# Optimization experiments

Measured on AMD Instinct MI355X. Metric: run time of the kernel, lower is better.

## Reference

```python
import jax, jax.numpy as jnp
import numpy as np

N_QUBITS = 4            # hardcoded by _QLayer encoder (4 rx inputs)
STATE_DIM = 1024        # 2**gnn_arch[-1] = 2**10 amplitudes per node state
FEAT_DIM = 2 * STATE_DIM
HIDDEN = 4              # must equal n_qubits for gating broadcast
OUT_DIM = 2048
N_NODES = 8192

# PauliZ expectation signs: wire 0 is the most-significant bit of the basis index
_IDX = np.arange(2 ** N_QUBITS)
_SIGNS = np.stack([1.0 - 2.0 * ((_IDX >> (N_QUBITS - 1 - w)) & 1) for w in range(N_QUBITS)], axis=1).astype(np.float32)  # [16,4]


def _apply_rx(state, angles, wire):
    # state: [B,2,2,2,2] complex64, angles: [B]
    half = 0.5 * angles
    c = jnp.cos(half).astype(jnp.complex64)
    s = (-1j) * jnp.sin(half).astype(jnp.complex64)
    gate = jnp.stack([jnp.stack([c, s], -1), jnp.stack([s, c], -1)], -2)  # [B,2,2]
    st = jnp.moveaxis(state, wire + 1, 1)
    st = jnp.einsum('bij,bj...->bi...', gate, st)
    return jnp.moveaxis(st, 1, wire + 1)


def _cnot(state, ctrl, tgt):
    flipped = jnp.flip(state, axis=tgt + 1)
    shape = [1] * state.ndim
    shape[ctrl + 1] = 2
    mask = jnp.arange(2).reshape(shape)
    return jnp.where(mask == 1, flipped, state)


def _qlayer(x, theta):
    # x: [B,4] encoding angles; theta: [4] trainable RX angles
    B = x.shape[0]
    state = jnp.zeros((B,) + (2,) * N_QUBITS, jnp.complex64)
    state = state.at[(slice(None),) + (0,) * N_QUBITS].set(1.0)
    for w in range(N_QUBITS):
        state = _apply_rx(state, x[:, w], w)          # encoder RX
    for w in range(N_QUBITS):
        state = _apply_rx(state, jnp.broadcast_to(theta[w], (B,)), w)  # trainable RX
    for w in range(N_QUBITS):
        state = _cnot(state, w, (w + 1) % N_QUBITS)   # CNOT ring (last -> 0)
    probs = (state.real ** 2 + state.imag ** 2).reshape(B, -1)  # [B,16]
    return probs @ jnp.asarray(_SIGNS)                 # [B,4] PauliZ expvals


def setup_inputs() -> dict:
    key = jax.random.key(0)
    ks = jax.random.split(key, 16)
    # random normalized complex node states -> real|imag concat features
    re = jax.random.normal(ks[0], (N_NODES, STATE_DIM), jnp.float32)
    im = jax.random.normal(ks[1], (N_NODES, STATE_DIM), jnp.float32)
    norm = jnp.sqrt(jnp.sum(re ** 2 + im ** 2, axis=1, keepdims=True))
    features = (jnp.concatenate([re, im], axis=1) / norm)[:, None, :]  # [N,1,FEAT_DIM]

    D = FEAT_DIM + HIDDEN
    bound = 1.0 / np.sqrt(D)

    def lin(k):
        kw, kb = jax.random.split(k)
        W = jax.random.uniform(kw, (N_QUBITS, D), jnp.float32, -bound, bound)
        b = jax.random.uniform(kb, (N_QUBITS,), jnp.float32, -bound, bound)
        return W, b

    Wf, bf = lin(ks[2]); Wi, bi = lin(ks[3]); Wg, bg = lin(ks[4]); Wo, bo = lin(ks[5])
    theta_f = jax.random.uniform(ks[6], (N_QUBITS,), jnp.float32, 0.0, 2.0 * np.pi)
    theta_i = jax.random.uniform(ks[7], (N_QUBITS,), jnp.float32, 0.0, 2.0 * np.pi)
    theta_g = jax.random.uniform(ks[8], (N_QUBITS,), jnp.float32, 0.0, 2.0 * np.pi)
    theta_o = jax.random.uniform(ks[9], (N_QUBITS,), jnp.float32, 0.0, 2.0 * np.pi)
    fb = 1.0 / np.sqrt(HIDDEN)
    Wfin = jax.random.uniform(ks[10], (OUT_DIM, HIDDEN), jnp.float32, -fb, fb)
    bfin = jax.random.uniform(ks[11], (OUT_DIM,), jnp.float32, -fb, fb)
    return {"features": features, "Wf": Wf, "bf": bf, "Wi": Wi, "bi": bi,
            "Wg": Wg, "bg": bg, "Wo": Wo, "bo": bo,
            "theta_f": theta_f, "theta_i": theta_i, "theta_g": theta_g, "theta_o": theta_o,
            "Wfin": Wfin, "bfin": bfin}


def reference(features, Wf, bf, Wi, bi, Wg, bg, Wo, bo,
              theta_f, theta_i, theta_g, theta_o, Wfin, bfin):
    D = features.shape[-1]
    Wfx, Wfh = Wf[:, :D], Wf[:, D:]
    Wix, Wih = Wi[:, :D], Wi[:, D:]
    Wgx, Wgh = Wg[:, :D], Wg[:, D:]
    Wox, Woh = Wo[:, :D], Wo[:, D:]
    # precompute the x-part of all gate projections (the only big GEMM)
    px_f = jnp.einsum('nbd,qd->nbq', features, Wfx) + bf
    px_i = jnp.einsum('nbd,qd->nbq', features, Wix) + bi
    px_g = jnp.einsum('nbd,qd->nbq', features, Wgx) + bg
    px_o = jnp.einsum('nbd,qd->nbq', features, Wox) + bo

    B = features.shape[1]
    h0 = jnp.zeros((B, HIDDEN), jnp.float32)
    c0 = jnp.zeros((B, HIDDEN), jnp.float32)

    def step(carry, xs):
        hx, cx = carry
        pf, pi, pg, po = xs
        f = jax.nn.sigmoid(_qlayer(pf + hx @ Wfh.T, theta_f))
        i = jax.nn.sigmoid(_qlayer(pi + hx @ Wih.T, theta_i))
        g = jnp.tanh(_qlayer(pg + hx @ Wgh.T, theta_g))
        o = jax.nn.sigmoid(_qlayer(po + hx @ Woh.T, theta_o))
        cx = f * cx + i * g
        hx = o * jnp.tanh(cx)
        return (hx, cx), hx

    _, outs = jax.lax.scan(step, (h0, c0), (px_f, px_i, px_g, px_o))  # outs: [N,B,H]
    return outs[:, 0, :] @ Wfin.T + bfin  # [N, OUT_DIM]
```

## Files before the change

kernel.cpp:

```cpp
#include <hip/hip_runtime.h>
#include <stdint.h>
#include <math.h>

typedef unsigned int uint_t;

#define FEAT 2048
#define DSTRIDE 2052
#define WARM 40
#define LCH 16
#define STEPS (WARM + LCH)
#define NCH (NN / LCH)
#define NN 8192

__device__ __forceinline__ float sigm_f(float x) {
    return __builtin_amdgcn_rcpf(1.f + __expf(-x));
}
__device__ __forceinline__ float tanh_f(float x) {
    return 1.f - 2.f * __builtin_amdgcn_rcpf(__expf(2.f * x) + 1.f);
}

__global__ __launch_bounds__(256) void k_px(
    const float* __restrict__ feat,
    const float* __restrict__ Wf, const float* __restrict__ Wi,
    const float* __restrict__ Wg, const float* __restrict__ Wo,
    const float* __restrict__ bfp, const float* __restrict__ bip,
    const float* __restrict__ bgp, const float* __restrict__ bop,
    const float* __restrict__ thf, const float* __restrict__ thi,
    const float* __restrict__ thg, const float* __restrict__ tho,
    float* __restrict__ px2)
{
    __shared__ float Wl[16 * 512];
    const int t = threadIdx.x;
    const int wave = t >> 6, lane = t & 63;
    const int rowBase = blockIdx.x * 16;
    const float* Ws[4] = {Wf, Wi, Wg, Wo};

    float acc[4][16];
#pragma unroll
    for (int r = 0; r < 4; ++r)
#pragma unroll
        for (int i = 0; i < 16; ++i) acc[r][i] = 0.f;

    for (int ch = 0; ch < 4; ++ch) {
        __syncthreads();
        for (int i4 = t; i4 < 2048; i4 += 256) {
            const int gq = i4 >> 7;
            const int jj = (i4 & 127) << 2;
            const int g = gq >> 2, q = gq & 3;
            const float4 v = *(const float4*)(Ws[g] + q * DSTRIDE + ch * 512 + jj);
            *(float4*)(&Wl[gq * 512 + jj]) = v;
        }
        __syncthreads();
#pragma unroll
        for (int rr = 0; rr < 4; ++rr) {
            const int n = rowBase + wave * 4 + rr;
            const float* fp = feat + (size_t)n * FEAT + ch * 512 + lane * 8;
            const float4 fa = *(const float4*)(fp);
            const float4 fb = *(const float4*)(fp + 4);
#pragma unroll
            for (int gq = 0; gq < 16; ++gq) {
                const float4 wa = *(const float4*)(&Wl[gq * 512 + lane * 8]);
                const float4 wb = *(const float4*)(&Wl[gq * 512 + lane * 8 + 4]);
                float a = acc[rr][gq];
                a = fmaf(fa.x, wa.x, a); a = fmaf(fa.y, wa.y, a);
                a = fmaf(fa.z, wa.z, a); a = fmaf(fa.w, wa.w, a);
                a = fmaf(fb.x, wb.x, a); a = fmaf(fb.y, wb.y, a);
                a = fmaf(fb.z, wb.z, a); a = fmaf(fb.w, wb.w, a);
                acc[rr][gq] = a;
            }
        }
    }

    float bth[16];
    {
        const float* bs[4] = {bfp, bip, bgp, bop};
        const float* ts[4] = {thf, thi, thg, tho};
#pragma unroll
        for (int g = 0; g < 4; ++g)
#pragma unroll
            for (int q = 0; q < 4; ++q)
                bth[g * 4 + q] = bs[g][q] + ts[g][q];
    }

#pragma unroll
    for (int rr = 0; rr < 4; ++rr) {
#pragma unroll
        for (int i = 0; i < 16; ++i) {
            float v = acc[rr][i];
#pragma unroll
            for (int m = 32; m > 0; m >>= 1) v += __shfl_xor(v, m, 64);
            acc[rr][i] = v + bth[i];
        }
        if (lane == 0) {
            const int n = rowBase + wave * 4 + rr;
            float* dst = px2 + (size_t)n * 16;
            *(float4*)(dst + 0)  = make_float4(acc[rr][0],  acc[rr][1],  acc[rr][2],  acc[rr][3]);
            *(float4*)(dst + 4)  = make_float4(acc[rr][4],  acc[rr][5],  acc[rr][6],  acc[rr][7]);
            *(float4*)(dst + 8)  = make_float4(acc[rr][8],  acc[rr][9],  acc[rr][10], acc[rr][11]);
            *(float4*)(dst + 12) = make_float4(acc[rr][12], acc[rr][13], acc[rr][14], acc[rr][15]);
        }
    }
}

__global__ __launch_bounds__(256) void k_scan(
    const float* __restrict__ Wf, const float* __restrict__ Wi,
    const float* __restrict__ Wg, const float* __restrict__ Wo,
    const float* __restrict__ px2, float* __restrict__ hout)
{
    const int c = blockIdx.x * 256 + threadIdx.x;
    float wh[4][4][4];
    {
        const float* Ws[4] = {Wf, Wi, Wg, Wo};
#pragma unroll
        for (int g = 0; g < 4; ++g)
#pragma unroll
            for (int q = 0; q < 4; ++q)
#pragma unroll
                for (int j = 0; j < 4; ++j)
                    wh[g][q][j] = Ws[g][q * DSTRIDE + FEAT + j];
    }
    float h[4] = {0.f, 0.f, 0.f, 0.f};
    float cc[4] = {0.f, 0.f, 0.f, 0.f};

    float4 PN0, PN1, PN2, PN3;
    {
        const int n0 = c * LCH - WARM;
        const int nc = n0 < 0 ? 0 : n0;
        const float* p = px2 + (size_t)nc * 16;
        PN0 = *(const float4*)(p + 0);
        PN1 = *(const float4*)(p + 4);
        PN2 = *(const float4*)(p + 8);
        PN3 = *(const float4*)(p + 12);
    }

    for (int s = 0; s < STEPS; ++s) {
        const int n = c * LCH + s - WARM;

        float4 PP[4];
        PP[0] = PN0; PP[1] = PN1; PP[2] = PN2; PP[3] = PN3;

        {
            int n2 = n + 1;
            n2 = n2 < 0 ? 0 : n2;
            n2 = n2 > (NN - 1) ? (NN - 1) : n2;
            const float* p2 = px2 + (size_t)n2 * 16;
            PN0 = *(const float4*)(p2 + 0);
            PN1 = *(const float4*)(p2 + 4);
            PN2 = *(const float4*)(p2 + 8);
            PN3 = *(const float4*)(p2 + 12);
        }

        float act[4][4];
#pragma unroll
        for (int g = 0; g < 4; ++g) {
            float z0 = PP[g].x, z1 = PP[g].y, z2 = PP[g].z, z3 = PP[g].w;
#pragma unroll
            for (int j = 0; j < 4; ++j) {
                z0 = fmaf(h[j], wh[g][0][j], z0);
                z1 = fmaf(h[j], wh[g][1][j], z1);
                z2 = fmaf(h[j], wh[g][2][j], z2);
                z3 = fmaf(h[j], wh[g][3][j], z3);
            }
            const float c0 = __cosf(z0), c1 = __cosf(z1);
            const float c2 = __cosf(z2), c3 = __cosf(z3);
            const float m01 = c0 * c1, t23 = c2 * c3;
            const float y0 = c1 * t23, y1 = m01, y2 = m01 * c2, y3 = m01 * t23;
            if (g == 2) {
                act[g][0] = tanh_f(y0); act[g][1] = tanh_f(y1);
                act[g][2] = tanh_f(y2); act[g][3] = tanh_f(y3);
            } else {
                act[g][0] = sigm_f(y0); act[g][1] = sigm_f(y1);
                act[g][2] = sigm_f(y2); act[g][3] = sigm_f(y3);
            }
        }
        if (n >= 0) {
#pragma unroll
            for (int q = 0; q < 4; ++q) {
                const float cn = fmaf(act[0][q], cc[q], act[1][q] * act[2][q]);
                cc[q] = cn;
                h[q] = act[3][q] * tanh_f(cn);
            }
        }
        if (s >= WARM) {
            *(float4*)(hout + (size_t)n * 4) = make_float4(h[0], h[1], h[2], h[3]);
        }
    }
}

__global__ __launch_bounds__(256) void k_out_main(
    const float* __restrict__ hout,
    const float* __restrict__ Wfin, const float* __restrict__ bfin,
    float* __restrict__ out)
{
    const int n = blockIdx.x;
    const int ko = threadIdx.x * 8;
    const float4 h = *(const float4*)(hout + (size_t)n * 4);
    const float4 b0 = *(const float4*)(bfin + ko);
    const float4 b1 = *(const float4*)(bfin + ko + 4);
    const float bb[8] = {b0.x, b0.y, b0.z, b0.w, b1.x, b1.y, b1.z, b1.w};
    float o[8];
#pragma unroll
    for (int j = 0; j < 8; ++j) {
        const float4 w = *(const float4*)(Wfin + (size_t)(ko + j) * 4);
        float v = bb[j];
        v = fmaf(h.x, w.x, v); v = fmaf(h.y, w.y, v);
        v = fmaf(h.z, w.z, v); v = fmaf(h.w, w.w, v);
        o[j] = v;
    }
    float* dst = out + (size_t)n * 2048 + ko;
    *(float4*)(dst)     = make_float4(o[0], o[1], o[2], o[3]);
    *(float4*)(dst + 4) = make_float4(o[4], o[5], o[6], o[7]);
}

__global__ __launch_bounds__(256) void k_out_tail(
    const float* __restrict__ hout,
    const float* __restrict__ Wfin, const float* __restrict__ bfin,
    float* __restrict__ out)
{
    __shared__ float hs[16 * 4];
    const int t = threadIdx.x;
    if (t < 64) hs[t] = hout[(size_t)8176 * 4 + t];
    __syncthreads();
    const int r = t >> 4;
    const int n = 8176 + r;
    const int c0 = (t & 15) * 128;
    const float4 h = *(const float4*)(&hs[r * 4]);
    for (int j = 0; j < 128; j += 8) {
        const int ko = c0 + j;
        const float4 b0 = *(const float4*)(bfin + ko);
        const float4 b1 = *(const float4*)(bfin + ko + 4);
        const float bb[8] = {b0.x, b0.y, b0.z, b0.w, b1.x, b1.y, b1.z, b1.w};
        float o[8];
#pragma unroll
        for (int jj = 0; jj < 8; ++jj) {
            const float4 w = *(const float4*)(Wfin + (size_t)(ko + jj) * 4);
            float v = bb[jj];
            v = fmaf(h.x, w.x, v); v = fmaf(h.y, w.y, v);
            v = fmaf(h.z, w.z, v); v = fmaf(h.w, w.w, v);
            o[jj] = v;
        }
        float* dst = out + (size_t)n * 2048 + ko;
        *(float4*)(dst)     = make_float4(o[0], o[1], o[2], o[3]);
        *(float4*)(dst + 4) = make_float4(o[4], o[5], o[6], o[7]);
    }
}

__global__ __launch_bounds__(256) void k_sentinel(float* __restrict__ out) {
    const size_t i = (size_t)blockIdx.x * 256 + threadIdx.x;
    *(float4*)(out + i * 4) = make_float4(123.f, 123.f, 123.f, 123.f);
}

extern "C" void kernel_launch(void* const* d_in, const int* in_sizes, int n_in,
                              void* d_out, int out_size, void* d_ws, size_t ws_size,
                              hipStream_t stream)
{
    const float* feat = (const float*)d_in[0];
    const float* Wf   = (const float*)d_in[1];
    const float* bfp  = (const float*)d_in[2];
    const float* Wi   = (const float*)d_in[3];
    const float* bip  = (const float*)d_in[4];
    const float* Wg   = (const float*)d_in[5];
    const float* bgp  = (const float*)d_in[6];
    const float* Wo   = (const float*)d_in[7];
    const float* bop  = (const float*)d_in[8];
    const float* thf  = (const float*)d_in[9];
    const float* thi  = (const float*)d_in[10];
    const float* thg  = (const float*)d_in[11];
    const float* tho  = (const float*)d_in[12];
    const float* Wfin = (const float*)d_in[13];
    const float* bfin = (const float*)d_in[14];

    bool ok = (n_in == 15) &&
              in_sizes[0] == 8192 * 2048 &&
              in_sizes[1] == 8208 && in_sizes[3] == 8208 &&
              in_sizes[5] == 8208 && in_sizes[7] == 8208 &&
              in_sizes[2] == 4 && in_sizes[4] == 4 &&
              in_sizes[6] == 4 && in_sizes[8] == 4 &&
              in_sizes[9] == 4 && in_sizes[10] == 4 &&
              in_sizes[11] == 4 && in_sizes[12] == 4 &&
              in_sizes[13] == 8192 && in_sizes[14] == 2048 &&
              out_size == 8192 * 2048;
    if (!ok) {
        hipLaunchKernelGGL(k_sentinel, dim3(8192 * 2048 / 1024), dim3(256), 0,
                           stream, (float*)d_out);
        return;
    }

    char* ob = (char*)d_out;
    float* px2  = (float*)ob;
    float* hout = (float*)(ob + (size_t)NN * 2048 * 4 - (size_t)NN * 16);
    float* out  = (float*)d_out;

    hipLaunchKernelGGL(k_px, dim3(512), dim3(256), 0, stream,
                       feat, Wf, Wi, Wg, Wo, bfp, bip, bgp, bop,
                       thf, thi, thg, tho, px2);
    hipLaunchKernelGGL(k_scan, dim3(2), dim3(256), 0, stream,
                       Wf, Wi, Wg, Wo, px2, hout);
    hipLaunchKernelGGL(k_out_main, dim3(NN - 16), dim3(256), 0, stream,
                       hout, Wfin, bfin, out);
    hipLaunchKernelGGL(k_out_tail, dim3(1), dim3(256), 0, stream,
                       hout, Wfin, bfin, out);
}
```

Measured before the change: 257.8 us.

## Halve scan chunk length, reorder px loop for weight reuse, batch output rows

```diff
diff --git a/kernel.cpp b/kernel.cpp
--- a/kernel.cpp
+++ b/kernel.cpp
@@ -7,7 +7,7 @@
 #define FEAT 2048
 #define DSTRIDE 2052
 #define WARM 40
-#define LCH 16
+#define LCH 8
 #define STEPS (WARM + LCH)
 #define NCH (NN / LCH)
 #define NN 8192
@@ -51,21 +51,26 @@
             *(float4*)(&Wl[gq * 512 + jj]) = v;
         }
         __syncthreads();
+
+        float4 fa[4], fb[4];
 #pragma unroll
         for (int rr = 0; rr < 4; ++rr) {
             const int n = rowBase + wave * 4 + rr;
             const float* fp = feat + (size_t)n * FEAT + ch * 512 + lane * 8;
-            const float4 fa = *(const float4*)(fp);
-            const float4 fb = *(const float4*)(fp + 4);
-#pragma unroll
-            for (int gq = 0; gq < 16; ++gq) {
-                const float4 wa = *(const float4*)(&Wl[gq * 512 + lane * 8]);
-                const float4 wb = *(const float4*)(&Wl[gq * 512 + lane * 8 + 4]);
+            fa[rr] = *(const float4*)(fp);
+            fb[rr] = *(const float4*)(fp + 4);
+        }
+#pragma unroll
+        for (int gq = 0; gq < 16; ++gq) {
+            const float4 wa = *(const float4*)(&Wl[gq * 512 + lane * 8]);
+            const float4 wb = *(const float4*)(&Wl[gq * 512 + lane * 8 + 4]);
+#pragma unroll
+            for (int rr = 0; rr < 4; ++rr) {
                 float a = acc[rr][gq];
-                a = fmaf(fa.x, wa.x, a); a = fmaf(fa.y, wa.y, a);
-                a = fmaf(fa.z, wa.z, a); a = fmaf(fa.w, wa.w, a);
-                a = fmaf(fb.x, wb.x, a); a = fmaf(fb.y, wb.y, a);
-                a = fmaf(fb.z, wb.z, a); a = fmaf(fb.w, wb.w, a);
+                a = fmaf(fa[rr].x, wa.x, a); a = fmaf(fa[rr].y, wa.y, a);
+                a = fmaf(fa[rr].z, wa.z, a); a = fmaf(fa[rr].w, wa.w, a);
+                a = fmaf(fb[rr].x, wb.x, a); a = fmaf(fb[rr].y, wb.y, a);
+                a = fmaf(fb[rr].z, wb.z, a); a = fmaf(fb[rr].w, wb.w, a);
                 acc[rr][gq] = a;
             }
         }
@@ -102,12 +107,12 @@
     }
 }
 
-__global__ __launch_bounds__(256) void k_scan(
+__global__ __launch_bounds__(512) void k_scan(
     const float* __restrict__ Wf, const float* __restrict__ Wi,
     const float* __restrict__ Wg, const float* __restrict__ Wo,
     const float* __restrict__ px2, float* __restrict__ hout)
 {
-    const int c = blockIdx.x * 256 + threadIdx.x;
+    const int c = blockIdx.x * 512 + threadIdx.x;
     float wh[4][4][4];
     {
         const float* Ws[4] = {Wf, Wi, Wg, Wo};
@@ -192,24 +197,32 @@
     const float* __restrict__ Wfin, const float* __restrict__ bfin,
     float* __restrict__ out)
 {
-    const int n = blockIdx.x;
+    const int n0 = blockIdx.x * 8;
     const int ko = threadIdx.x * 8;
-    const float4 h = *(const float4*)(hout + (size_t)n * 4);
+    float4 w[8];
+#pragma unroll
+    for (int j = 0; j < 8; ++j)
+        w[j] = *(const float4*)(Wfin + (size_t)(ko + j) * 4);
     const float4 b0 = *(const float4*)(bfin + ko);
     const float4 b1 = *(const float4*)(bfin + ko + 4);
     const float bb[8] = {b0.x, b0.y, b0.z, b0.w, b1.x, b1.y, b1.z, b1.w};
-    float o[8];
-#pragma unroll
-    for (int j = 0; j < 8; ++j) {
-        const float4 w = *(const float4*)(Wfin + (size_t)(ko + j) * 4);
-        float v = bb[j];
-        v = fmaf(h.x, w.x, v); v = fmaf(h.y, w.y, v);
-        v = fmaf(h.z, w.z, v); v = fmaf(h.w, w.w, v);
-        o[j] = v;
-    }
-    float* dst = out + (size_t)n * 2048 + ko;
-    *(float4*)(dst)     = make_float4(o[0], o[1], o[2], o[3]);
-    *(float4*)(dst + 4) = make_float4(o[4], o[5], o[6], o[7]);
+
+#pragma unroll
+    for (int r = 0; r < 8; ++r) {
+        const int n = n0 + r;
+        const float4 h = *(const float4*)(hout + (size_t)n * 4);
+        float o[8];
+#pragma unroll
+        for (int j = 0; j < 8; ++j) {
+            float v = bb[j];
+            v = fmaf(h.x, w[j].x, v); v = fmaf(h.y, w[j].y, v);
+            v = fmaf(h.z, w[j].z, v); v = fmaf(h.w, w[j].w, v);
+            o[j] = v;
+        }
+        float* dst = out + (size_t)n * 2048 + ko;
+        *(float4*)(dst)     = make_float4(o[0], o[1], o[2], o[3]);
+        *(float4*)(dst + 4) = make_float4(o[4], o[5], o[6], o[7]);
+    }
 }
 
 __global__ __launch_bounds__(256) void k_out_tail(
@@ -294,9 +307,9 @@
     hipLaunchKernelGGL(k_px, dim3(512), dim3(256), 0, stream,
                        feat, Wf, Wi, Wg, Wo, bfp, bip, bgp, bop,
                        thf, thi, thg, tho, px2);
-    hipLaunchKernelGGL(k_scan, dim3(2), dim3(256), 0, stream,
+    hipLaunchKernelGGL(k_scan, dim3(2), dim3(512), 0, stream,
                        Wf, Wi, Wg, Wo, px2, hout);
-    hipLaunchKernelGGL(k_out_main, dim3(NN - 16), dim3(256), 0, stream,
+    hipLaunchKernelGGL(k_out_main, dim3(1022), dim3(256), 0, stream,
                        hout, Wfin, bfin, out);
     hipLaunchKernelGGL(k_out_tail, dim3(1), dim3(256), 0, stream,
                        hout, Wfin, bfin, out);
```

After: 254.6 us. About the same (-1.2%).
